# Optimization experiments

Measured on AMD Instinct MI355X. Metric: run time of the kernel, lower is better.

The kernel has to match this reference:

```python
import jax, jax.numpy as jnp
import numpy as np

P_DROP = 0.6  # F.dropout default training=True in the original forward

def setup_inputs() -> dict:
    key = jax.random.key(0)
    k1, k2, k3, k4 = jax.random.split(key, 4)
    B, T, V, F, K, O = 32, 12, 1000, 64, 3, 64
    x = jax.random.normal(k1, (B, T, V, F), dtype=jnp.float32)
    Att = jax.random.uniform(k2, (V, V), dtype=jnp.float32)
    cheb = jax.random.normal(k3, (K, V, V), dtype=jnp.float32)   # Chebyshev polynomials T_k(L)
    Theta = jax.random.normal(k4, (K, F, O), dtype=jnp.float32)  # per-order feature transforms
    return {"x": x, "Att": Att, "cheb": cheb, "Theta": Theta}

def reference(x, Att, cheb, Theta):
    # x: [B,T,V,F]; Att: [V,V]; cheb: [K,V,V]; Theta: [K,F,O]
    B, T, V, F = x.shape
    K = cheb.shape[0]
    keep = 1.0 - P_DROP
    # Original draws a fresh dropout mask per (time_step, k); replicate with a fixed key.
    mask = jax.random.bernoulli(jax.random.key(42), keep, (T, K, V, V))
    TkA = cheb * Att                                   # [K,V,V] attention-weighted polynomial
    M = jnp.where(mask, TkA[None] / keep, 0.0)         # [T,K,V,V] inverted dropout
    # rhs = T_k_with_at @ graph_signal, batched over (b,t,k)
    rhs = jnp.einsum('tkuv,btvf->btkuf', M, x)         # [B,T,K,V,F]
    # sum_k rhs_k @ Theta_k  -> [B,T,V,O]; matches permute(0,3,1,2) of stacked outputs
    out = jnp.einsum('btkuf,kfo->btuo', rhs, Theta)
    return jax.nn.relu(out)
```

## Files before the change

kernel.cpp:

```cpp
#include <hip/hip_runtime.h>
#include <hip/hip_bf16.h>
#include <stdint.h>


typedef __attribute__((ext_vector_type(8))) short short8;
typedef __attribute__((ext_vector_type(4))) float f32x4;

__device__ __forceinline__ ushort f2bf(float f) {
  __hip_bfloat16 h = __float2bfloat16(f);
  return *reinterpret_cast<ushort*>(&h);
}

__device__ __forceinline__ void threefry2x32(uint32_t c0, uint32_t c1,
                                             uint32_t& o0, uint32_t& o1) {
  const uint32_t ks0 = 0u;
  const uint32_t ks1 = 42u;
  const uint32_t ks2 = ks0 ^ ks1 ^ 0x1BD11BDAu;
  uint32_t x0 = c0 + ks0;
  uint32_t x1 = c1 + ks1;
#define TFR(r) { x0 += x1; x1 = (x1 << (r)) | (x1 >> (32 - (r))); x1 ^= x0; }
  TFR(13) TFR(15) TFR(26) TFR(6)
  x0 += ks1; x1 += ks2 + 1u;
  TFR(17) TFR(29) TFR(16) TFR(24)
  x0 += ks2; x1 += ks0 + 2u;
  TFR(13) TFR(15) TFR(26) TFR(6)
  x0 += ks0; x1 += ks1 + 3u;
  TFR(17) TFR(29) TFR(16) TFR(24)
  x0 += ks1; x1 += ks2 + 4u;
  TFR(13) TFR(15) TFR(26) TFR(6)
  x0 += ks2; x1 += ks0 + 5u;
#undef TFR
  o0 = x0; o1 = x1;
}

__global__ void prep(const float* __restrict__ x,
                     const float* __restrict__ Att,
                     const float* __restrict__ cheb,
                     ushort* __restrict__ Mws,
                     ushort* __restrict__ xtw) {
  __shared__ float lt[64][65];
  const int bid = blockIdx.x;
  const int tid = threadIdx.x;

  if (bid >= 6144) {
    const uint32_t idx = (uint32_t)(bid - 6144) * 256u + tid;
    const uint32_t vp = idx & 1023u;
    const uint32_t up = (idx >> 10) & 1023u;
    const uint32_t tk = idx >> 20;
    float val = 0.f;
    if ((vp < 1000u) & (up < 1000u)) {
      const uint32_t flat = (tk * 1000u + up) * 1000u + vp;
      uint32_t o0, o1;
      threefry2x32(0u, flat, o0, o1);
      const uint32_t bits = o0 ^ o1;
      const float u = __uint_as_float((bits >> 9) | 0x3f800000u) - 1.0f;
      if (u < 0.4f) {
        val = cheb[(tk % 3u) * 1000000u + up * 1000u + vp] *
              Att[up * 1000u + vp] * 2.5f;
      }
    }
    Mws[idx] = f2bf(val);
    return;
  }

  const int r = bid;
  const int vc = r & 15, t = (r >> 4) % 12, b = r / 192;
  const int v0 = vc * 64;
#pragma unroll
  for (int i = 0; i < 4; ++i) {
    const int c = i * 256 + tid;
    const int vi = c >> 4, f4 = c & 15;
    float4 q = make_float4(0.f, 0.f, 0.f, 0.f);
    if (v0 + vi < 1000)
      q = *(const float4*)(x + ((((size_t)b * 12 + t) * 1000 + v0 + vi) << 6) + f4 * 4);
    lt[f4 * 4 + 0][vi] = q.x;
    lt[f4 * 4 + 1][vi] = q.y;
    lt[f4 * 4 + 2][vi] = q.z;
    lt[f4 * 4 + 3][vi] = q.w;
  }
  __syncthreads();
  const int f = tid >> 2, g = tid & 3;
  alignas(16) ushort tmp[16];
#pragma unroll
  for (int j = 0; j < 16; ++j) tmp[j] = f2bf(lt[f][g * 16 + j]);
  const size_t base = ((size_t)(t * 2048 + b * 64 + f)) << 10;
  *(uint4*)(xtw + base + v0 + g * 16)     = *(const uint4*)&tmp[0];
  *(uint4*)(xtw + base + v0 + g * 16 + 8) = *(const uint4*)&tmp[8];
}

#define LDT 72
#define MFMA(a, b, c) __builtin_amdgcn_mfma_f32_16x16x32_bf16((a), (b), (c), 0, 0, 0)

#define LOADCH(VC)                                                            \
  do {                                                                        \
    const size_t co_ = (size_t)(VC) * 64;                                     \
    p0 = *(const uint4*)(Mws + aS0 + co_);                                    \
    p1 = *(const uint4*)(Mws + aS1 + co_);                                    \
    p2 = *(const uint4*)(Mws + aS2 + co_);                                    \
    p3 = *(const uint4*)(Mws + aS3 + co_);                                    \
    p4 = *(const uint4*)(Mws + aS4 + co_);                                    \
    p5 = *(const uint4*)(Mws + aS5 + co_);                                    \
    p6 = *(const uint4*)(xt + bS0 + co_);                                     \
    p7 = *(const uint4*)(xt + bS1 + co_);                                     \
    p8 = *(const uint4*)(xt + bS2 + co_);                                     \
    p9 = *(const uint4*)(xt + bS3 + co_);                                     \
  } while (0)

#define WRITECH(BP)                                                           \
  do {                                                                        \
    *(uint4*)&(BP)[(tid) * 8]                = p0;                            \
    *(uint4*)&(BP)[(256 + tid) * 8]          = p1;                            \
    *(uint4*)&(BP)[(512 + tid) * 8]          = p2;                            \
    *(uint4*)&(BP)[(768 + tid) * 8]          = p3;                            \
    *(uint4*)&(BP)[(1024 + tid) * 8]         = p4;                            \
    *(uint4*)&(BP)[(1280 + tid) * 8]         = p5;                            \
    *(uint4*)&(BP)[12288 + (tid) * 8]        = p6;                            \
    *(uint4*)&(BP)[12288 + (256 + tid) * 8]  = p7;                            \
    *(uint4*)&(BP)[12288 + (512 + tid) * 8]  = p8;                            \
    *(uint4*)&(BP)[12288 + (768 + tid) * 8]  = p9;                            \
  } while (0)

#define BURST(BP)                                                             \
  do {                                                                        \
    _Pragma("unroll")                                                         \
    for (int ks = 0; ks < 2; ++ks) {                                          \
      const int cs_ = (((ks * 4 + quad) ^ rsw)) << 3;                         \
      short8 bv[4];                                                           \
      _Pragma("unroll")                                                       \
      for (int ni = 0; ni < 4; ++ni)                                          \
        bv[ni] = *(const short8*)&(BP)[12288 +                                \
                     (wn * 64 + ni * 16 + l15) * 64 + cs_];                   \
      _Pragma("unroll")                                                       \
      for (int k = 0; k < 3; ++k) {                                           \
        short8 av[2];                                                         \
        _Pragma("unroll")                                                     \
        for (int mi = 0; mi < 2; ++mi)                                        \
          av[mi] = *(const short8*)&(BP)[k * 4096 +                           \
                       (wu * 32 + mi * 16 + l15) * 64 + cs_];                 \
        _Pragma("unroll")                                                     \
        for (int mi = 0; mi < 2; ++mi)                                        \
          _Pragma("unroll")                                                   \
          for (int ni = 0; ni < 4; ++ni)                                      \
            pacc[k][mi][ni] = MFMA(av[mi], bv[ni], pacc[k][mi][ni]);          \
      }                                                                       \
    }                                                                         \
  } while (0)

__global__ __launch_bounds__(256, 2)
void cheb_main(const ushort* __restrict__ Mws, const ushort* __restrict__ xt,
               const float* __restrict__ Theta, float* __restrict__ out) {
  __shared__ __align__(16) ushort smem[40960];
  const int tid = threadIdx.x;
  const int lane = tid & 63;
  const int w = tid >> 6;
  const int wu = w >> 1, wn = w & 1;
  const int quad = lane >> 4, l15 = lane & 15;
  const int rsw = l15 & 7;

  ushort* buf0 = smem;
  ushort* buf1 = smem + 20480;

  const int bid = blockIdx.x;
  const int swz = (bid & 7) * 384 + (bid >> 3);
  const int ut = swz & 15;
  const int g = swz >> 4;
  const int nt = g & 15;
  const int t = g >> 4;
  const int u0 = ut * 64, n0 = nt * 128;

  const size_t mbase = (size_t)(t * 3) << 20;
  const size_t xrow0 = (size_t)(t * 2048 + n0);

  const int rA0 = tid >> 3,              cA0 = (tid & 7) ^ (rA0 & 7);
  const int rA1 = ((256 + tid) >> 3) & 63, cA1 = (tid & 7) ^ (rA1 & 7);
  const size_t aS0 = mbase + ((size_t)(u0 + rA0) << 10) + cA0 * 8;
  const size_t aS1 = mbase + ((size_t)(u0 + rA1) << 10) + cA1 * 8;
  const size_t aS2 = mbase + (1ull << 20) + ((size_t)(u0 + rA0) << 10) + cA0 * 8;
  const size_t aS3 = mbase + (1ull << 20) + ((size_t)(u0 + rA1) << 10) + cA1 * 8;
  const size_t aS4 = mbase + (2ull << 20) + ((size_t)(u0 + rA0) << 10) + cA0 * 8;
  const size_t aS5 = mbase + (2ull << 20) + ((size_t)(u0 + rA1) << 10) + cA1 * 8;
  const int rB0 = tid >> 3,         cB0 = (tid & 7) ^ (rB0 & 7);
  const int rB1 = (256 + tid) >> 3, cB1 = (tid & 7) ^ (rB1 & 7);
  const int rB2 = (512 + tid) >> 3, cB2 = (tid & 7) ^ (rB2 & 7);
  const int rB3 = (768 + tid) >> 3, cB3 = (tid & 7) ^ (rB3 & 7);
  const size_t bS0 = ((xrow0 + rB0) << 10) + cB0 * 8;
  const size_t bS1 = ((xrow0 + rB1) << 10) + cB1 * 8;
  const size_t bS2 = ((xrow0 + rB2) << 10) + cB2 * 8;
  const size_t bS3 = ((xrow0 + rB3) << 10) + cB3 * 8;

  f32x4 pacc[3][2][4];
#pragma unroll
  for (int k = 0; k < 3; ++k)
#pragma unroll
    for (int i = 0; i < 2; ++i)
#pragma unroll
      for (int j = 0; j < 4; ++j) pacc[k][i][j] = f32x4{0.f, 0.f, 0.f, 0.f};

  uint4 p0, p1, p2, p3, p4, p5, p6, p7, p8, p9;

  LOADCH(0);
  WRITECH(buf0);
  __syncthreads();

#pragma unroll 1
  for (int it = 0; it < 8; ++it) {
    const int vc = it * 2;
    if (vc < 15) LOADCH(vc + 1);
    __builtin_amdgcn_s_setprio(1);
    BURST(buf0);
    __builtin_amdgcn_s_setprio(0);
    if (vc < 15) WRITECH(buf1);
    __syncthreads();
    if (vc + 1 < 15) LOADCH(vc + 2);
    __builtin_amdgcn_s_setprio(1);
    BURST(buf1);
    __builtin_amdgcn_s_setprio(0);
    if (vc + 1 < 15) WRITECH(buf0);
    __syncthreads();
  }

  ushort* sP  = smem + w * 2304;
  ushort* sTh = smem + 9216;
  f32x4 oacc[2][4];
#pragma unroll
  for (int i = 0; i < 2; ++i)
#pragma unroll
    for (int j = 0; j < 4; ++j) oacc[i][j] = f32x4{0.f, 0.f, 0.f, 0.f};

#pragma unroll
  for (int k = 0; k < 3; ++k) {
    __syncthreads();
#pragma unroll
    for (int mi = 0; mi < 2; ++mi)
#pragma unroll
      for (int ni = 0; ni < 4; ++ni)
#pragma unroll
        for (int r = 0; r < 4; ++r)
          sP[(mi * 16 + quad * 4 + r) * LDT + ni * 16 + l15] = f2bf(pacc[k][mi][ni][r]);
    for (int e = tid; e < 4096; e += 256) {
      const int f = e >> 6, o = e & 63;
      sTh[o * LDT + f] = f2bf(Theta[k * 4096 + e]);
    }
    __syncthreads();
#pragma unroll
    for (int ks = 0; ks < 2; ++ks) {
      short8 a2[2], b2[4];
#pragma unroll
      for (int mi = 0; mi < 2; ++mi)
        a2[mi] = *(const short8*)&sP[(mi * 16 + l15) * LDT + ks * 32 + quad * 8];
#pragma unroll
      for (int ni = 0; ni < 4; ++ni)
        b2[ni] = *(const short8*)&sTh[(ni * 16 + l15) * LDT + ks * 32 + quad * 8];
#pragma unroll
      for (int mi = 0; mi < 2; ++mi)
#pragma unroll
        for (int ni = 0; ni < 4; ++ni)
          oacc[mi][ni] = MFMA(a2[mi], b2[ni], oacc[mi][ni]);
    }
  }

#pragma unroll
  for (int mi = 0; mi < 2; ++mi) {
    const int u_base = u0 + wu * 32 + mi * 16 + quad * 4;
#pragma unroll
    for (int ni = 0; ni < 4; ++ni) {
      const int n = n0 + wn * 64 + ni * 16 + l15;
      const int b = n >> 6, oo = n & 63;
      float* op = out + (((size_t)b * 12 + t) * 1000) * 64 + oo;
#pragma unroll
      for (int r = 0; r < 4; ++r) {
        const int u = u_base + r;
        if (u < 1000) op[(size_t)u * 64] = fmaxf(oacc[mi][ni][r], 0.f);
      }
    }
  }
}

extern "C" void kernel_launch(void* const* d_in, const int* in_sizes, int n_in,
                              void* d_out, int out_size, void* d_ws, size_t ws_size,
                              hipStream_t stream) {
  const float* x     = (const float*)d_in[0];
  const float* Att   = (const float*)d_in[1];
  const float* cheb  = (const float*)d_in[2];
  const float* Theta = (const float*)d_in[3];
  float* out = (float*)d_out;

  ushort* Mws = (ushort*)d_ws;
  ushort* xtw = Mws + 37748736ull;

  prep<<<153600, 256, 0, stream>>>(x, Att, cheb, Mws, xtw);
  cheb_main<<<3072, 256, 0, stream>>>(Mws, xtw, Theta, out);
}
```

Before: 277.3 us.

## Prepack dropout matrix in MFMA fragment order and load A directly to registers

The prep kernel now writes the masked Chebyshev-attention matrix in an order that matches the per-lane MFMA A-fragment layout. The main kernel then loads A operands straight from global memory into registers instead of staging them through LDS. This cuts LDS traffic and LDS footprint, since only the x tile is double-buffered in shared memory. In exchange, A loads are no longer prefetched a stage ahead, so global latency may be exposed right before each burst, and register pressure rises.

Result: no change. 272.5 us (-1.8%).

```diff
diff --git a/kernel.cpp b/kernel.cpp
--- a/kernel.cpp
+++ b/kernel.cpp
@@ -36,7 +36,7 @@
 __global__ void prep(const float* __restrict__ x,
                      const float* __restrict__ Att,
                      const float* __restrict__ cheb,
-                     ushort* __restrict__ Mws,
+                     ushort* __restrict__ Mf,
                      ushort* __restrict__ xtw) {
   __shared__ float lt[64][65];
   const int bid = blockIdx.x;
@@ -44,9 +44,14 @@
 
   if (bid >= 6144) {
     const uint32_t idx = (uint32_t)(bid - 6144) * 256u + tid;
-    const uint32_t vp = idx & 1023u;
-    const uint32_t up = (idx >> 10) & 1023u;
+    const uint32_t j = idx & 7u;
+    const uint32_t lane = (idx >> 3) & 63u;
+    const uint32_t ks = (idx >> 9) & 1u;
+    const uint32_t c = (idx >> 10) & 15u;
+    const uint32_t u16 = (idx >> 14) & 63u;
     const uint32_t tk = idx >> 20;
+    const uint32_t up = u16 * 16u + (lane & 15u);
+    const uint32_t vp = c * 64u + ks * 32u + (lane >> 4) * 8u + j;
     float val = 0.f;
     if ((vp < 1000u) & (up < 1000u)) {
       const uint32_t flat = (tk * 1000u + up) * 1000u + vp;
@@ -59,7 +64,7 @@
               Att[up * 1000u + vp] * 2.5f;
       }
     }
-    Mws[idx] = f2bf(val);
+    Mf[idx] = f2bf(val);
     return;
   }
 
@@ -91,33 +96,34 @@
 #define LDT 72
 #define MFMA(a, b, c) __builtin_amdgcn_mfma_f32_16x16x32_bf16((a), (b), (c), 0, 0, 0)
 
-#define LOADCH(VC)                                                            \
+#define LOADB(VC)                                                             \
   do {                                                                        \
     const size_t co_ = (size_t)(VC) * 64;                                     \
-    p0 = *(const uint4*)(Mws + aS0 + co_);                                    \
-    p1 = *(const uint4*)(Mws + aS1 + co_);                                    \
-    p2 = *(const uint4*)(Mws + aS2 + co_);                                    \
-    p3 = *(const uint4*)(Mws + aS3 + co_);                                    \
-    p4 = *(const uint4*)(Mws + aS4 + co_);                                    \
-    p5 = *(const uint4*)(Mws + aS5 + co_);                                    \
     p6 = *(const uint4*)(xt + bS0 + co_);                                     \
     p7 = *(const uint4*)(xt + bS1 + co_);                                     \
     p8 = *(const uint4*)(xt + bS2 + co_);                                     \
     p9 = *(const uint4*)(xt + bS3 + co_);                                     \
   } while (0)
 
-#define WRITECH(BP)                                                           \
-  do {                                                                        \
-    *(uint4*)&(BP)[(tid) * 8]                = p0;                            \
-    *(uint4*)&(BP)[(256 + tid) * 8]          = p1;                            \
-    *(uint4*)&(BP)[(512 + tid) * 8]          = p2;                            \
-    *(uint4*)&(BP)[(768 + tid) * 8]          = p3;                            \
-    *(uint4*)&(BP)[(1024 + tid) * 8]         = p4;                            \
-    *(uint4*)&(BP)[(1280 + tid) * 8]         = p5;                            \
-    *(uint4*)&(BP)[12288 + (tid) * 8]        = p6;                            \
-    *(uint4*)&(BP)[12288 + (256 + tid) * 8]  = p7;                            \
-    *(uint4*)&(BP)[12288 + (512 + tid) * 8]  = p8;                            \
-    *(uint4*)&(BP)[12288 + (768 + tid) * 8]  = p9;                            \
+#define WRITEB(BP)                                                            \
+  do {                                                                        \
+    *(uint4*)&(BP)[(tid) * 8]        = p6;                                    \
+    *(uint4*)&(BP)[(256 + tid) * 8]  = p7;                                    \
+    *(uint4*)&(BP)[(512 + tid) * 8]  = p8;                                    \
+    *(uint4*)&(BP)[(768 + tid) * 8]  = p9;                                    \
+  } while (0)
+
+#define LOADA(VC)                                                             \
+  do {                                                                        \
+    const size_t co_ = (size_t)(VC) << 10;                                    \
+    _Pragma("unroll")                                                         \
+    for (int k = 0; k < 3; ++k)                                               \
+      _Pragma("unroll")                                                       \
+      for (int mi = 0; mi < 2; ++mi)                                          \
+        _Pragma("unroll")                                                     \
+        for (int ks = 0; ks < 2; ++ks)                                        \
+          a[k][mi][ks] = *(const short8*)(Mf + fA[k][mi] + co_ +              \
+                                          ((size_t)ks << 9));                 \
   } while (0)
 
 #define BURST(BP)                                                             \
@@ -128,28 +134,21 @@
       short8 bv[4];                                                           \
       _Pragma("unroll")                                                       \
       for (int ni = 0; ni < 4; ++ni)                                          \
-        bv[ni] = *(const short8*)&(BP)[12288 +                                \
-                     (wn * 64 + ni * 16 + l15) * 64 + cs_];                   \
+        bv[ni] = *(const short8*)&(BP)[(wn * 64 + ni * 16 + l15) * 64 + cs_]; \
       _Pragma("unroll")                                                       \
-      for (int k = 0; k < 3; ++k) {                                           \
-        short8 av[2];                                                         \
-        _Pragma("unroll")                                                     \
-        for (int mi = 0; mi < 2; ++mi)                                        \
-          av[mi] = *(const short8*)&(BP)[k * 4096 +                           \
-                       (wu * 32 + mi * 16 + l15) * 64 + cs_];                 \
+      for (int k = 0; k < 3; ++k)                                             \
         _Pragma("unroll")                                                     \
         for (int mi = 0; mi < 2; ++mi)                                        \
           _Pragma("unroll")                                                   \
           for (int ni = 0; ni < 4; ++ni)                                      \
-            pacc[k][mi][ni] = MFMA(av[mi], bv[ni], pacc[k][mi][ni]);          \
-      }                                                                       \
+            pacc[k][mi][ni] = MFMA(a[k][mi][ks], bv[ni], pacc[k][mi][ni]);    \
     }                                                                         \
   } while (0)
 
 __global__ __launch_bounds__(256, 2)
-void cheb_main(const ushort* __restrict__ Mws, const ushort* __restrict__ xt,
+void cheb_main(const ushort* __restrict__ Mf, const ushort* __restrict__ xt,
                const float* __restrict__ Theta, float* __restrict__ out) {
-  __shared__ __align__(16) ushort smem[40960];
+  __shared__ __align__(16) ushort smem[16384];
   const int tid = threadIdx.x;
   const int lane = tid & 63;
   const int w = tid >> 6;
@@ -158,7 +157,7 @@
   const int rsw = l15 & 7;
 
   ushort* buf0 = smem;
-  ushort* buf1 = smem + 20480;
+  ushort* buf1 = smem + 8192;
 
   const int bid = blockIdx.x;
   const int swz = (bid & 7) * 384 + (bid >> 3);
@@ -168,17 +167,15 @@
   const int t = g >> 4;
   const int u0 = ut * 64, n0 = nt * 128;
 
-  const size_t mbase = (size_t)(t * 3) << 20;
+  size_t fA[3][2];
+#pragma unroll
+  for (int k = 0; k < 3; ++k)
+#pragma unroll
+    for (int mi = 0; mi < 2; ++mi)
+      fA[k][mi] = (((size_t)((t * 3 + k) * 64 + ut * 4 + wu * 2 + mi)) << 14)
+                  + (size_t)lane * 8;
+
   const size_t xrow0 = (size_t)(t * 2048 + n0);
-
-  const int rA0 = tid >> 3,              cA0 = (tid & 7) ^ (rA0 & 7);
-  const int rA1 = ((256 + tid) >> 3) & 63, cA1 = (tid & 7) ^ (rA1 & 7);
-  const size_t aS0 = mbase + ((size_t)(u0 + rA0) << 10) + cA0 * 8;
-  const size_t aS1 = mbase + ((size_t)(u0 + rA1) << 10) + cA1 * 8;
-  const size_t aS2 = mbase + (1ull << 20) + ((size_t)(u0 + rA0) << 10) + cA0 * 8;
-  const size_t aS3 = mbase + (1ull << 20) + ((size_t)(u0 + rA1) << 10) + cA1 * 8;
-  const size_t aS4 = mbase + (2ull << 20) + ((size_t)(u0 + rA0) << 10) + cA0 * 8;
-  const size_t aS5 = mbase + (2ull << 20) + ((size_t)(u0 + rA1) << 10) + cA1 * 8;
   const int rB0 = tid >> 3,         cB0 = (tid & 7) ^ (rB0 & 7);
   const int rB1 = (256 + tid) >> 3, cB1 = (tid & 7) ^ (rB1 & 7);
   const int rB2 = (512 + tid) >> 3, cB2 = (tid & 7) ^ (rB2 & 7);
@@ -196,26 +193,29 @@
 #pragma unroll
       for (int j = 0; j < 4; ++j) pacc[k][i][j] = f32x4{0.f, 0.f, 0.f, 0.f};
 
-  uint4 p0, p1, p2, p3, p4, p5, p6, p7, p8, p9;
-
-  LOADCH(0);
-  WRITECH(buf0);
+  short8 a[3][2][2];
+  uint4 p6, p7, p8, p9;
+
+  LOADB(0);
+  WRITEB(buf0);
   __syncthreads();
 
 #pragma unroll 1
   for (int it = 0; it < 8; ++it) {
     const int vc = it * 2;
-    if (vc < 15) LOADCH(vc + 1);
+    if (vc < 15) LOADB(vc + 1);
+    LOADA(vc);
     __builtin_amdgcn_s_setprio(1);
     BURST(buf0);
     __builtin_amdgcn_s_setprio(0);
-    if (vc < 15) WRITECH(buf1);
-    __syncthreads();
-    if (vc + 1 < 15) LOADCH(vc + 2);
+    if (vc < 15) WRITEB(buf1);
+    __syncthreads();
+    if (vc + 1 < 15) LOADB(vc + 2);
+    LOADA(vc + 1);
     __builtin_amdgcn_s_setprio(1);
     BURST(buf1);
     __builtin_amdgcn_s_setprio(0);
-    if (vc + 1 < 15) WRITECH(buf0);
+    if (vc + 1 < 15) WRITEB(buf0);
     __syncthreads();
   }
 
@@ -285,9 +285,9 @@
   const float* Theta = (const float*)d_in[3];
   float* out = (float*)d_out;
 
-  ushort* Mws = (ushort*)d_ws;
-  ushort* xtw = Mws + 37748736ull;
-
-  prep<<<153600, 256, 0, stream>>>(x, Att, cheb, Mws, xtw);
-  cheb_main<<<3072, 256, 0, stream>>>(Mws, xtw, Theta, out);
-}
+  ushort* Mf  = (ushort*)d_ws;
+  ushort* xtw = Mf + 37748736ull;
+
+  prep<<<153600, 256, 0, stream>>>(x, Att, cheb, Mf, xtw);
+  cheb_main<<<3072, 256, 0, stream>>>(Mf, xtw, Theta, out);
+}
```

## Store dropout-masked operator in MFMA fragment order for direct LDS reads

Applied to the files above, without the earlier changes.

The prep kernel now writes the masked bf16 operator M in a pre-tiled layout that matches the MFMA A-fragment lane order: 16-row groups, k-halves and per-lane 8-element chunks. The main kernel's A tiles are then fetched as contiguous per-wave chunks and read from LDS with a simple lane*8 stride instead of a swizzled row/column index. This is meant to cut address arithmetic and bank conflicts on A-operand LDS reads and to make global loads fully contiguous. The cost is a more complex index computation in prep's scattered writes and a layout tied to this MFMA shape.

New measurement: 329.5 us. 18.8% more time.

```diff
diff --git a/kernel.cpp b/kernel.cpp
--- a/kernel.cpp
+++ b/kernel.cpp
@@ -36,7 +36,7 @@
 __global__ void prep(const float* __restrict__ x,
                      const float* __restrict__ Att,
                      const float* __restrict__ cheb,
-                     ushort* __restrict__ Mws,
+                     ushort* __restrict__ Mf,
                      ushort* __restrict__ xtw) {
   __shared__ float lt[64][65];
   const int bid = blockIdx.x;
@@ -44,9 +44,14 @@
 
   if (bid >= 6144) {
     const uint32_t idx = (uint32_t)(bid - 6144) * 256u + tid;
-    const uint32_t vp = idx & 1023u;
-    const uint32_t up = (idx >> 10) & 1023u;
+    const uint32_t j = idx & 7u;
+    const uint32_t lane = (idx >> 3) & 63u;
+    const uint32_t ks = (idx >> 9) & 1u;
+    const uint32_t c = (idx >> 10) & 15u;
+    const uint32_t u16 = (idx >> 14) & 63u;
     const uint32_t tk = idx >> 20;
+    const uint32_t up = u16 * 16u + (lane & 15u);
+    const uint32_t vp = c * 64u + ks * 32u + (lane >> 4) * 8u + j;
     float val = 0.f;
     if ((vp < 1000u) & (up < 1000u)) {
       const uint32_t flat = (tk * 1000u + up) * 1000u + vp;
@@ -59,7 +64,7 @@
               Att[up * 1000u + vp] * 2.5f;
       }
     }
-    Mws[idx] = f2bf(val);
+    Mf[idx] = f2bf(val);
     return;
   }
 
@@ -93,31 +98,32 @@
 
 #define LOADCH(VC)                                                            \
   do {                                                                        \
-    const size_t co_ = (size_t)(VC) * 64;                                     \
-    p0 = *(const uint4*)(Mws + aS0 + co_);                                    \
-    p1 = *(const uint4*)(Mws + aS1 + co_);                                    \
-    p2 = *(const uint4*)(Mws + aS2 + co_);                                    \
-    p3 = *(const uint4*)(Mws + aS3 + co_);                                    \
-    p4 = *(const uint4*)(Mws + aS4 + co_);                                    \
-    p5 = *(const uint4*)(Mws + aS5 + co_);                                    \
-    p6 = *(const uint4*)(xt + bS0 + co_);                                     \
-    p7 = *(const uint4*)(xt + bS1 + co_);                                     \
-    p8 = *(const uint4*)(xt + bS2 + co_);                                     \
-    p9 = *(const uint4*)(xt + bS3 + co_);                                     \
+    const size_t coA_ = (size_t)(VC) << 10;                                   \
+    const size_t coB_ = (size_t)(VC) * 64;                                    \
+    pA0 = *(const uint4*)(Mf + aS[0] + coA_);                                 \
+    pA1 = *(const uint4*)(Mf + aS[1] + coA_);                                 \
+    pA2 = *(const uint4*)(Mf + aS[2] + coA_);                                 \
+    pA3 = *(const uint4*)(Mf + aS[3] + coA_);                                 \
+    pA4 = *(const uint4*)(Mf + aS[4] + coA_);                                 \
+    pA5 = *(const uint4*)(Mf + aS[5] + coA_);                                 \
+    pB0 = *(const uint4*)(xt + bS0 + coB_);                                   \
+    pB1 = *(const uint4*)(xt + bS1 + coB_);                                   \
+    pB2 = *(const uint4*)(xt + bS2 + coB_);                                   \
+    pB3 = *(const uint4*)(xt + bS3 + coB_);                                   \
   } while (0)
 
 #define WRITECH(BP)                                                           \
   do {                                                                        \
-    *(uint4*)&(BP)[(tid) * 8]                = p0;                            \
-    *(uint4*)&(BP)[(256 + tid) * 8]          = p1;                            \
-    *(uint4*)&(BP)[(512 + tid) * 8]          = p2;                            \
-    *(uint4*)&(BP)[(768 + tid) * 8]          = p3;                            \
-    *(uint4*)&(BP)[(1024 + tid) * 8]         = p4;                            \
-    *(uint4*)&(BP)[(1280 + tid) * 8]         = p5;                            \
-    *(uint4*)&(BP)[12288 + (tid) * 8]        = p6;                            \
-    *(uint4*)&(BP)[12288 + (256 + tid) * 8]  = p7;                            \
-    *(uint4*)&(BP)[12288 + (512 + tid) * 8]  = p8;                            \
-    *(uint4*)&(BP)[12288 + (768 + tid) * 8]  = p9;                            \
+    *(uint4*)&(BP)[(tid) * 8]                 = pA0;                          \
+    *(uint4*)&(BP)[(256 + tid) * 8]           = pA1;                          \
+    *(uint4*)&(BP)[(512 + tid) * 8]           = pA2;                          \
+    *(uint4*)&(BP)[(768 + tid) * 8]           = pA3;                          \
+    *(uint4*)&(BP)[(1024 + tid) * 8]          = pA4;                          \
+    *(uint4*)&(BP)[(1280 + tid) * 8]          = pA5;                          \
+    *(uint4*)&(BP)[12288 + (tid) * 8]         = pB0;                          \
+    *(uint4*)&(BP)[12288 + (256 + tid) * 8]   = pB1;                          \
+    *(uint4*)&(BP)[12288 + (512 + tid) * 8]   = pB2;                          \
+    *(uint4*)&(BP)[12288 + (768 + tid) * 8]   = pB3;                          \
   } while (0)
 
 #define BURST(BP)                                                             \
@@ -135,8 +141,8 @@
         short8 av[2];                                                         \
         _Pragma("unroll")                                                     \
         for (int mi = 0; mi < 2; ++mi)                                        \
-          av[mi] = *(const short8*)&(BP)[k * 4096 +                           \
-                       (wu * 32 + mi * 16 + l15) * 64 + cs_];                 \
+          av[mi] = *(const short8*)&(BP)[                                     \
+                       (k * 8 + (wu * 2 + mi) * 2 + ks) * 512 + lane * 8];    \
         _Pragma("unroll")                                                     \
         for (int mi = 0; mi < 2; ++mi)                                        \
           _Pragma("unroll")                                                   \
@@ -147,7 +153,7 @@
   } while (0)
 
 __global__ __launch_bounds__(256, 2)
-void cheb_main(const ushort* __restrict__ Mws, const ushort* __restrict__ xt,
+void cheb_main(const ushort* __restrict__ Mf, const ushort* __restrict__ xt,
                const float* __restrict__ Theta, float* __restrict__ out) {
   __shared__ __align__(16) ushort smem[40960];
   const int tid = threadIdx.x;
@@ -168,17 +174,16 @@
   const int t = g >> 4;
   const int u0 = ut * 64, n0 = nt * 128;
 
-  const size_t mbase = (size_t)(t * 3) << 20;
+  size_t aS[6];
+#pragma unroll
+  for (int i = 0; i < 6; ++i) {
+    const int f = i * 4 + w;
+    const int k = f >> 3, u16g = (f & 7) >> 1, ks = f & 1;
+    aS[i] = (((size_t)((t * 3 + k) * 64 + ut * 4 + u16g)) << 14)
+            + (size_t)ks * 512 + (size_t)lane * 8;
+  }
+
   const size_t xrow0 = (size_t)(t * 2048 + n0);
-
-  const int rA0 = tid >> 3,              cA0 = (tid & 7) ^ (rA0 & 7);
-  const int rA1 = ((256 + tid) >> 3) & 63, cA1 = (tid & 7) ^ (rA1 & 7);
-  const size_t aS0 = mbase + ((size_t)(u0 + rA0) << 10) + cA0 * 8;
-  const size_t aS1 = mbase + ((size_t)(u0 + rA1) << 10) + cA1 * 8;
-  const size_t aS2 = mbase + (1ull << 20) + ((size_t)(u0 + rA0) << 10) + cA0 * 8;
-  const size_t aS3 = mbase + (1ull << 20) + ((size_t)(u0 + rA1) << 10) + cA1 * 8;
-  const size_t aS4 = mbase + (2ull << 20) + ((size_t)(u0 + rA0) << 10) + cA0 * 8;
-  const size_t aS5 = mbase + (2ull << 20) + ((size_t)(u0 + rA1) << 10) + cA1 * 8;
   const int rB0 = tid >> 3,         cB0 = (tid & 7) ^ (rB0 & 7);
   const int rB1 = (256 + tid) >> 3, cB1 = (tid & 7) ^ (rB1 & 7);
   const int rB2 = (512 + tid) >> 3, cB2 = (tid & 7) ^ (rB2 & 7);
@@ -196,7 +201,7 @@
 #pragma unroll
       for (int j = 0; j < 4; ++j) pacc[k][i][j] = f32x4{0.f, 0.f, 0.f, 0.f};
 
-  uint4 p0, p1, p2, p3, p4, p5, p6, p7, p8, p9;
+  uint4 pA0, pA1, pA2, pA3, pA4, pA5, pB0, pB1, pB2, pB3;
 
   LOADCH(0);
   WRITECH(buf0);
@@ -285,9 +290,9 @@
   const float* Theta = (const float*)d_in[3];
   float* out = (float*)d_out;
 
-  ushort* Mws = (ushort*)d_ws;
-  ushort* xtw = Mws + 37748736ull;
-
-  prep<<<153600, 256, 0, stream>>>(x, Att, cheb, Mws, xtw);
-  cheb_main<<<3072, 256, 0, stream>>>(Mws, xtw, Theta, out);
-}
+  ushort* Mf  = (ushort*)d_ws;
+  ushort* xtw = Mf + 37748736ull;
+
+  prep<<<153600, 256, 0, stream>>>(x, Att, cheb, Mf, xtw);
+  cheb_main<<<3072, 256, 0, stream>>>(Mf, xtw, Theta, out);
+}
```
